# Optimization experiments

Measured on AMD Instinct MI355X. Metric: run time of the kernel, lower is better.

## Reference

```python
import jax, jax.numpy as jnp
import numpy as np

N = 50000   # nodes
E = 800000  # edges (avg degree 16)
D = 128     # in_dim == out_dim
EPS = 1e-5  # LayerNorm eps (torch default)


def setup_inputs() -> dict:
    key = jax.random.key(0)
    ks = jax.random.split(key, 8)
    x = jax.random.normal(ks[0], (N, D), dtype=jnp.float32)
    edge_row = jax.random.randint(ks[1], (E,), 0, N, dtype=jnp.int32)
    edge_col = jax.random.randint(ks[2], (E,), 0, N, dtype=jnp.int32)
    edge_val = jax.random.uniform(ks[3], (E,), dtype=jnp.float32)
    W = jax.random.normal(ks[4], (D, D), dtype=jnp.float32) / np.sqrt(D).astype(np.float32)
    b = jnp.zeros((D,), jnp.float32)
    gamma = jnp.ones((D,), jnp.float32)
    beta = jnp.zeros((D,), jnp.float32)
    return {"x": x, "edge_val": edge_val, "W": W, "b": b,
            "gamma": gamma, "beta": beta,
            "edge_row": edge_row, "edge_col": edge_col}


def reference(x, edge_val, W, b, gamma, beta, edge_row, edge_col):
    # SpMM: support = adj @ x, adj in COO form (row, col, val)
    msgs = edge_val[:, None] * x[edge_col]                      # [E, D] gather
    support = jax.ops.segment_sum(msgs, edge_row, num_segments=x.shape[0])  # [N, D]
    # Linear (torch stores weight as [out, in])
    h = support @ W.T + b                                       # [N, D]
    # LayerNorm over last dim
    mu = jnp.mean(h, axis=-1, keepdims=True)
    var = jnp.mean(jnp.square(h - mu), axis=-1, keepdims=True)
    h = (h - mu) * jax.lax.rsqrt(var + EPS) * gamma + beta
    # ReLU; dropout is identity at inference
    return jax.nn.relu(h)
```

## Files before the change

### kernel.cpp

```cpp
#include <hip/hip_runtime.h>

#define D 128
#define LN_EPS 1e-5f
#define RPB 16
#define POISON 0xAAAAAAAAu
#define BINSTRIDE 4864
#define SBF_STRIDE 68
#define ECAP 68
#define EMAX 64
#define P1BLOCKS 512
#define CURSTRIDE 16

typedef __attribute__((ext_vector_type(8))) short short8;
typedef __attribute__((ext_vector_type(4))) float f32x4;

union FragU { uint4 u; short8 s; };

__device__ __forceinline__ unsigned bf16_hi(float f) {
    unsigned u = __float_as_uint(f);
    return (u + 0x7FFFu + ((u >> 16) & 1u)) & 0xFFFF0000u;
}
__device__ __forceinline__ float lo16f(unsigned u) { return __uint_as_float(u << 16); }
__device__ __forceinline__ float hi16f(unsigned u) { return __uint_as_float(u & 0xFFFF0000u); }

__global__ void __launch_bounds__(256) prep1_kernel(
    const int* __restrict__ edge_row, const int* __restrict__ edge_col,
    const float* __restrict__ edge_val,
    const float* __restrict__ W, const float* __restrict__ x,
    unsigned* __restrict__ Wb, unsigned* __restrict__ xb16,
    unsigned* __restrict__ bin_cursor, uint2* __restrict__ binbuf,
    int E, int n8, int nbins, int epb) {
    __shared__ int cntL[256];
    __shared__ int curL[256];
    __shared__ int baseL[256];
    int t = threadIdx.x;
    int gid = blockIdx.x * 256 + t;
    int gsz = gridDim.x * 256;

    cntL[t] = 0;

    if (gid < 8192) {
        int u  = gid & 3;
        int L  = (gid >> 2) & 63;
        int nt = (gid >> 8) & 7;
        int kt = gid >> 11;
        int n = nt * 16 + (L & 15);
        int k = kt * 32 + (L >> 4) * 8 + u * 2;
        unsigned lo = bf16_hi(W[n * D + k]) >> 16;
        unsigned hi = bf16_hi(W[n * D + k + 1]);
        Wb[gid] = hi | lo;
    }

    for (int j = gid; j < n8; j += gsz) {
        float4 a = *(const float4*)(x + (size_t)j * 8);
        float4 c = *(const float4*)(x + (size_t)j * 8 + 4);
        uint4 o;
        o.x = bf16_hi(a.y) | (bf16_hi(a.x) >> 16);
        o.y = bf16_hi(a.w) | (bf16_hi(a.z) >> 16);
        o.z = bf16_hi(c.y) | (bf16_hi(c.x) >> 16);
        o.w = bf16_hi(c.w) | (bf16_hi(c.z) >> 16);
        *(uint4*)(xb16 + (size_t)j * 4) = o;
    }
    __syncthreads();

    int e0 = blockIdx.x * epb;
    int e1 = e0 + epb; if (e1 > E) e1 = E;

    {
        int i = e0 + t * 4;
        for (; i + 3 < e1; i += 1024) {
            int4 r = *(const int4*)(edge_row + i);
            atomicAdd(&cntL[r.x >> 8], 1);
            atomicAdd(&cntL[r.y >> 8], 1);
            atomicAdd(&cntL[r.z >> 8], 1);
            atomicAdd(&cntL[r.w >> 8], 1);
        }
        for (; i < e1; ++i) atomicAdd(&cntL[edge_row[i] >> 8], 1);
    }
    __syncthreads();
    if (t < nbins) {
        int c = cntL[t];
        baseL[t] = c ? (int)(atomicAdd(&bin_cursor[t * CURSTRIDE], (unsigned)c) - POISON) : 0;
    }
    curL[t] = 0;
    __syncthreads();

    {
        int i = e0 + t * 4;
        for (; i + 3 < e1; i += 1024) {
            int4 r = *(const int4*)(edge_row + i);
            int4 c = *(const int4*)(edge_col + i);
            float4 v = *(const float4*)(edge_val + i);
            int b0 = r.x >> 8, b1 = r.y >> 8, b2 = r.z >> 8, b3 = r.w >> 8;
            int p0 = atomicAdd(&curL[b0], 1) + baseL[b0];
            int p1 = atomicAdd(&curL[b1], 1) + baseL[b1];
            int p2 = atomicAdd(&curL[b2], 1) + baseL[b2];
            int p3 = atomicAdd(&curL[b3], 1) + baseL[b3];
            if (p0 < BINSTRIDE)
                binbuf[(size_t)b0 * BINSTRIDE + p0] =
                    make_uint2(((unsigned)c.x << 16) | (unsigned)(r.x & 255), bf16_hi(v.x));
            if (p1 < BINSTRIDE)
                binbuf[(size_t)b1 * BINSTRIDE + p1] =
                    make_uint2(((unsigned)c.y << 16) | (unsigned)(r.y & 255), bf16_hi(v.y));
            if (p2 < BINSTRIDE)
                binbuf[(size_t)b2 * BINSTRIDE + p2] =
                    make_uint2(((unsigned)c.z << 16) | (unsigned)(r.z & 255), bf16_hi(v.z));
            if (p3 < BINSTRIDE)
                binbuf[(size_t)b3 * BINSTRIDE + p3] =
                    make_uint2(((unsigned)c.w << 16) | (unsigned)(r.w & 255), bf16_hi(v.w));
        }
        for (; i < e1; ++i) {
            int r = edge_row[i];
            int bin = r >> 8;
            int p = atomicAdd(&curL[bin], 1) + baseL[bin];
            if (p < BINSTRIDE)
                binbuf[(size_t)bin * BINSTRIDE + p] =
                    make_uint2(((unsigned)edge_col[i] << 16) | (unsigned)(r & 255),
                               bf16_hi(edge_val[i]));
        }
    }
}

__global__ void __launch_bounds__(256) fused_gather_linear(
    const unsigned* __restrict__ xb16, const uint2* __restrict__ binbuf,
    const unsigned* __restrict__ bin_cursor, const unsigned* __restrict__ Wb,
    const float* __restrict__ b, const float* __restrict__ gamma,
    const float* __restrict__ beta, float* __restrict__ out, int N) {
    __shared__ unsigned ecol[RPB][ECAP];
    __shared__ int ecnt[RPB];
    __shared__ int pdeg[RPB];
    __shared__ unsigned sbf[RPB][SBF_STRIDE];
    __shared__ float sh[RPB][D];
    __shared__ float mu_s[RPB], inv_s[RPB];
    int t = threadIdx.x;

    int nwg = (int)gridDim.x;
    int swq = nwg >> 3, swr = nwg & 7;
    int xcd = (int)blockIdx.x & 7;
    int logical = (xcd < swr ? xcd * (swq + 1) : swr * (swq + 1) + (xcd - swr) * swq)
                + ((int)blockIdx.x >> 3);
    int row0 = logical * RPB;
    int bin  = logical >> 4;
    int tb   = (logical & 15) * RPB;

    if (t < RPB) ecnt[t] = 0;
    int sz = (int)(bin_cursor[bin * CURSTRIDE] - POISON);
    if (sz > BINSTRIDE) sz = BINSTRIDE;
    if (sz < 0) sz = 0;
    const uint2* bb = binbuf + (size_t)bin * BINSTRIDE;
    __syncthreads();

    {
        int half = sz >> 1;
        for (int i = t; i < half; i += 256) {
            uint4 two = *(const uint4*)(bb + (size_t)2 * i);
            int rl0 = (int)(two.x & 255u) - tb;
            if ((unsigned)rl0 < RPB) {
                int p = atomicAdd(&ecnt[rl0], 1);
                if (p < EMAX) ecol[rl0][p] = two.y | (two.x >> 16);
            }
            int rl1 = (int)(two.z & 255u) - tb;
            if ((unsigned)rl1 < RPB) {
                int p = atomicAdd(&ecnt[rl1], 1);
                if (p < EMAX) ecol[rl1][p] = two.w | (two.z >> 16);
            }
        }
        if (t == 0 && (sz & 1)) {
            uint2 rec = bb[sz - 1];
            int rl = (int)(rec.x & 255u) - tb;
            if ((unsigned)rl < RPB) {
                int p = atomicAdd(&ecnt[rl], 1);
                if (p < EMAX) ecol[rl][p] = rec.y | (rec.x >> 16);
            }
        }
    }
    __syncthreads();
    if (t < RPB) {
        int c = ecnt[t]; if (c > EMAX) c = EMAX;
        int pe = (c + 3) & ~3;
        for (int k = c; k < pe; ++k) ecol[t][k] = 0;
        pdeg[t] = pe;
    }
    __syncthreads();

    {
        int r = t >> 4;
        int qd = t & 15;
        int row = row0 + r;
        float4 accA = make_float4(0.f, 0.f, 0.f, 0.f);
        float4 accB = make_float4(0.f, 0.f, 0.f, 0.f);
        if (row < N) {
            int pd = pdeg[r];
            const unsigned* xb = xb16 + qd * 4;
            for (int e = 0; e < pd; e += 4) {
                uint4 p = *(const uint4*)&ecol[r][e];
                unsigned c0 = p.x & 0xFFFFu, c1 = p.y & 0xFFFFu;
                unsigned c2 = p.z & 0xFFFFu, c3 = p.w & 0xFFFFu;
                float w0 = __uint_as_float(p.x & 0xFFFF0000u);
                float w1 = __uint_as_float(p.y & 0xFFFF0000u);
                float w2 = __uint_as_float(p.z & 0xFFFF0000u);
                float w3 = __uint_as_float(p.w & 0xFFFF0000u);
                uint4 X0 = *(const uint4*)(xb + (size_t)c0 * (D / 2));
                uint4 X1 = *(const uint4*)(xb + (size_t)c1 * (D / 2));
                uint4 X2 = *(const uint4*)(xb + (size_t)c2 * (D / 2));
                uint4 X3 = *(const uint4*)(xb + (size_t)c3 * (D / 2));
                accA.x = fmaf(w0, lo16f(X0.x), accA.x);
                accA.y = fmaf(w0, hi16f(X0.x), accA.y);
                accA.z = fmaf(w0, lo16f(X0.y), accA.z);
                accA.w = fmaf(w0, hi16f(X0.y), accA.w);
                accB.x = fmaf(w0, lo16f(X0.z), accB.x);
                accB.y = fmaf(w0, hi16f(X0.z), accB.y);
                accB.z = fmaf(w0, lo16f(X0.w), accB.z);
                accB.w = fmaf(w0, hi16f(X0.w), accB.w);
                accA.x = fmaf(w1, lo16f(X1.x), accA.x);
                accA.y = fmaf(w1, hi16f(X1.x), accA.y);
                accA.z = fmaf(w1, lo16f(X1.y), accA.z);
                accA.w = fmaf(w1, hi16f(X1.y), accA.w);
                accB.x = fmaf(w1, lo16f(X1.z), accB.x);
                accB.y = fmaf(w1, hi16f(X1.z), accB.y);
                accB.z = fmaf(w1, lo16f(X1.w), accB.z);
                accB.w = fmaf(w1, hi16f(X1.w), accB.w);
                accA.x = fmaf(w2, lo16f(X2.x), accA.x);
                accA.y = fmaf(w2, hi16f(X2.x), accA.y);
                accA.z = fmaf(w2, lo16f(X2.y), accA.z);
                accA.w = fmaf(w2, hi16f(X2.y), accA.w);
                accB.x = fmaf(w2, lo16f(X2.z), accB.x);
                accB.y = fmaf(w2, hi16f(X2.z), accB.y);
                accB.z = fmaf(w2, lo16f(X2.w), accB.z);
                accB.w = fmaf(w2, hi16f(X2.w), accB.w);
                accA.x = fmaf(w3, lo16f(X3.x), accA.x);
                accA.y = fmaf(w3, hi16f(X3.x), accA.y);
                accA.z = fmaf(w3, lo16f(X3.y), accA.z);
                accA.w = fmaf(w3, hi16f(X3.y), accA.w);
                accB.x = fmaf(w3, lo16f(X3.z), accB.x);
                accB.y = fmaf(w3, hi16f(X3.z), accB.y);
                accB.z = fmaf(w3, lo16f(X3.w), accB.z);
                accB.w = fmaf(w3, hi16f(X3.w), accB.w);
            }
        }
        uint4 o;
        o.x = bf16_hi(accA.y) | (bf16_hi(accA.x) >> 16);
        o.y = bf16_hi(accA.w) | (bf16_hi(accA.z) >> 16);
        o.z = bf16_hi(accB.y) | (bf16_hi(accB.x) >> 16);
        o.w = bf16_hi(accB.w) | (bf16_hi(accB.z) >> 16);
        *(uint4*)&sbf[r][qd * 4] = o;
    }
    __syncthreads();

    {
        int L = t & 63;
        int w = t >> 6;
        int m = L & 15;
        int g = L >> 4;
        f32x4 acc0 = {0.f, 0.f, 0.f, 0.f};
        f32x4 acc1 = {0.f, 0.f, 0.f, 0.f};
#pragma unroll
        for (int kt = 0; kt < 4; ++kt) {
            FragU a, b0, b1;
            a.u  = *(const uint4*)&sbf[m][kt * 16 + g * 4];
            b0.u = *(const uint4*)(Wb + (((size_t)(kt * 8 + w * 2)) * 64 + L) * 4);
            b1.u = *(const uint4*)(Wb + (((size_t)(kt * 8 + w * 2 + 1)) * 64 + L) * 4);
            acc0 = __builtin_amdgcn_mfma_f32_16x16x32_bf16(a.s, b0.s, acc0, 0, 0, 0);
            acc1 = __builtin_amdgcn_mfma_f32_16x16x32_bf16(a.s, b1.s, acc1, 0, 0, 0);
        }
        int n0 = w * 32 + m;
        int n1 = n0 + 16;
        float bv0 = b[n0], bv1 = b[n1];
#pragma unroll
        for (int i = 0; i < 4; ++i) {
            int rr = g * 4 + i;
            sh[rr][n0] = acc0[i] + bv0;
            sh[rr][n1] = acc1[i] + bv1;
        }
    }
    __syncthreads();

    {
        int rr = t >> 4, j = t & 15;
        float sum = 0.f, sq = 0.f;
#pragma unroll
        for (int i = 0; i < 8; ++i) {
            float v = sh[rr][j + 16 * i];
            sum += v;
            sq = fmaf(v, v, sq);
        }
#pragma unroll
        for (int off = 8; off > 0; off >>= 1) {
            sum += __shfl_down(sum, off, 16);
            sq  += __shfl_down(sq, off, 16);
        }
        if (j == 0) {
            float mu = sum * (1.0f / D);
            float var = sq * (1.0f / D) - mu * mu;
            mu_s[rr] = mu;
            inv_s[rr] = rsqrtf(var + LN_EPS);
        }
    }
    __syncthreads();

    {
        int td = t & 127;
        int rbase = (t >> 7) * 8;
        float g = gamma[td], be = beta[td];
#pragma unroll
        for (int r = 0; r < 8; ++r) {
            int row = row0 + rbase + r;
            if (row < N) {
                float y = (sh[rbase + r][td] - mu_s[rbase + r]) * inv_s[rbase + r] * g + be;
                out[(size_t)row * D + td] = fmaxf(y, 0.f);
            }
        }
    }
}

extern "C" void kernel_launch(void* const* d_in, const int* in_sizes, int n_in,
                              void* d_out, int out_size, void* d_ws, size_t ws_size,
                              hipStream_t stream) {
    const float* x        = (const float*)d_in[0];
    const float* edge_val = (const float*)d_in[1];
    const float* W        = (const float*)d_in[2];
    const float* b        = (const float*)d_in[3];
    const float* gamma    = (const float*)d_in[4];
    const float* beta     = (const float*)d_in[5];
    const int*   edge_row = (const int*)d_in[6];
    const int*   edge_col = (const int*)d_in[7];

    const int N = in_sizes[0] / D;
    const int E = in_sizes[1];
    const int n8 = N * D / 8;
    const int nbins = (N + 255) >> 8;

    char* ws = (char*)d_ws;
    uint2*    binbuf     = (uint2*)ws;     ws += (size_t)nbins * BINSTRIDE * sizeof(uint2);
    unsigned* xb16       = (unsigned*)ws;  ws += (size_t)N * (D / 2) * sizeof(unsigned);
    unsigned* Wb         = (unsigned*)ws;  ws += 8192 * sizeof(unsigned);
    unsigned* bin_cursor = (unsigned*)ws;  ws += 256 * CURSTRIDE * sizeof(unsigned);

    int epb = ((E + P1BLOCKS - 1) / P1BLOCKS + 3) & ~3;

    prep1_kernel<<<P1BLOCKS, 256, 0, stream>>>(edge_row, edge_col, edge_val,
                                               W, x, Wb, xb16, bin_cursor,
                                               binbuf, E, n8, nbins, epb);
    fused_gather_linear<<<(N + RPB - 1) / RPB, 256, 0, stream>>>(
        xb16, binbuf, bin_cursor, Wb, b, gamma, beta, (float*)d_out, N);
}
```

Before: 147.2 us.

## Bucket per-row edges by column range, widen prep blocks, pad LayerNorm buffer

```diff
diff --git a/kernel.cpp b/kernel.cpp
--- a/kernel.cpp
+++ b/kernel.cpp
@@ -6,9 +6,12 @@
 #define POISON 0xAAAAAAAAu
 #define BINSTRIDE 4864
 #define SBF_STRIDE 68
+#define SH_STRIDE 132
 #define ECAP 68
 #define EMAX 64
+#define NCH 8
 #define P1BLOCKS 512
+#define P1THREADS 1024
 #define CURSTRIDE 16
 
 typedef __attribute__((ext_vector_type(8))) short short8;
@@ -23,7 +26,7 @@
 __device__ __forceinline__ float lo16f(unsigned u) { return __uint_as_float(u << 16); }
 __device__ __forceinline__ float hi16f(unsigned u) { return __uint_as_float(u & 0xFFFF0000u); }
 
-__global__ void __launch_bounds__(256) prep1_kernel(
+__global__ void __launch_bounds__(P1THREADS) prep1_kernel(
     const int* __restrict__ edge_row, const int* __restrict__ edge_col,
     const float* __restrict__ edge_val,
     const float* __restrict__ W, const float* __restrict__ x,
@@ -34,10 +37,10 @@
     __shared__ int curL[256];
     __shared__ int baseL[256];
     int t = threadIdx.x;
-    int gid = blockIdx.x * 256 + t;
-    int gsz = gridDim.x * 256;
-
-    cntL[t] = 0;
+    int gid = blockIdx.x * P1THREADS + t;
+    int gsz = gridDim.x * P1THREADS;
+
+    if (t < 256) cntL[t] = 0;
 
     if (gid < 8192) {
         int u  = gid & 3;
@@ -68,7 +71,7 @@
 
     {
         int i = e0 + t * 4;
-        for (; i + 3 < e1; i += 1024) {
+        for (; i + 3 < e1; i += P1THREADS * 4) {
             int4 r = *(const int4*)(edge_row + i);
             atomicAdd(&cntL[r.x >> 8], 1);
             atomicAdd(&cntL[r.y >> 8], 1);
@@ -82,12 +85,12 @@
         int c = cntL[t];
         baseL[t] = c ? (int)(atomicAdd(&bin_cursor[t * CURSTRIDE], (unsigned)c) - POISON) : 0;
     }
-    curL[t] = 0;
+    if (t < 256) curL[t] = 0;
     __syncthreads();
 
     {
         int i = e0 + t * 4;
-        for (; i + 3 < e1; i += 1024) {
+        for (; i + 3 < e1; i += P1THREADS * 4) {
             int4 r = *(const int4*)(edge_row + i);
             int4 c = *(const int4*)(edge_col + i);
             float4 v = *(const float4*)(edge_val + i);
@@ -127,10 +130,12 @@
     const float* __restrict__ b, const float* __restrict__ gamma,
     const float* __restrict__ beta, float* __restrict__ out, int N) {
     __shared__ unsigned ecol[RPB][ECAP];
-    __shared__ int ecnt[RPB];
+    __shared__ int cnt2[RPB][NCH];
+    __shared__ int cur2[RPB][NCH];
+    __shared__ int base2[RPB][NCH];
     __shared__ int pdeg[RPB];
     __shared__ unsigned sbf[RPB][SBF_STRIDE];
-    __shared__ float sh[RPB][D];
+    __shared__ float sh[RPB][SH_STRIDE];
     __shared__ float mu_s[RPB], inv_s[RPB];
     int t = threadIdx.x;
 
@@ -143,11 +148,42 @@
     int bin  = logical >> 4;
     int tb   = (logical & 15) * RPB;
 
-    if (t < RPB) ecnt[t] = 0;
+    if (t < RPB * NCH) {
+        ((int*)cnt2)[t] = 0;
+        ((int*)cur2)[t] = 0;
+    }
     int sz = (int)(bin_cursor[bin * CURSTRIDE] - POISON);
     if (sz > BINSTRIDE) sz = BINSTRIDE;
     if (sz < 0) sz = 0;
     const uint2* bb = binbuf + (size_t)bin * BINSTRIDE;
+    __syncthreads();
+
+    {
+        int half = sz >> 1;
+        for (int i = t; i < half; i += 256) {
+            uint4 two = *(const uint4*)(bb + (size_t)2 * i);
+            int rl0 = (int)(two.x & 255u) - tb;
+            if ((unsigned)rl0 < RPB) atomicAdd(&cnt2[rl0][two.x >> 29], 1);
+            int rl1 = (int)(two.z & 255u) - tb;
+            if ((unsigned)rl1 < RPB) atomicAdd(&cnt2[rl1][two.z >> 29], 1);
+        }
+        if (t == 0 && (sz & 1)) {
+            unsigned xw = bb[sz - 1].x;
+            int rl = (int)(xw & 255u) - tb;
+            if ((unsigned)rl < RPB) atomicAdd(&cnt2[rl][xw >> 29], 1);
+        }
+    }
+    __syncthreads();
+
+    if (t < RPB) {
+        int base = 0;
+#pragma unroll
+        for (int c = 0; c < NCH; ++c) { base2[t][c] = base; base += cnt2[t][c]; }
+        int tot = base > EMAX ? EMAX : base;
+        int pe = (tot + 3) & ~3;
+        for (int k = tot; k < pe; ++k) ecol[t][k] = 0;
+        pdeg[t] = pe;
+    }
     __syncthreads();
 
     {
@@ -156,30 +192,26 @@
             uint4 two = *(const uint4*)(bb + (size_t)2 * i);
             int rl0 = (int)(two.x & 255u) - tb;
             if ((unsigned)rl0 < RPB) {
-                int p = atomicAdd(&ecnt[rl0], 1);
-                if (p < EMAX) ecol[rl0][p] = two.y | (two.x >> 16);
+                int ch = two.x >> 29;
+                int idx = base2[rl0][ch] + atomicAdd(&cur2[rl0][ch], 1);
+                if (idx < EMAX) ecol[rl0][idx] = two.y | (two.x >> 16);
             }
             int rl1 = (int)(two.z & 255u) - tb;
             if ((unsigned)rl1 < RPB) {
-                int p = atomicAdd(&ecnt[rl1], 1);
-                if (p < EMAX) ecol[rl1][p] = two.w | (two.z >> 16);
+                int ch = two.z >> 29;
+                int idx = base2[rl1][ch] + atomicAdd(&cur2[rl1][ch], 1);
+                if (idx < EMAX) ecol[rl1][idx] = two.w | (two.z >> 16);
             }
         }
         if (t == 0 && (sz & 1)) {
             uint2 rec = bb[sz - 1];
             int rl = (int)(rec.x & 255u) - tb;
             if ((unsigned)rl < RPB) {
-                int p = atomicAdd(&ecnt[rl], 1);
-                if (p < EMAX) ecol[rl][p] = rec.y | (rec.x >> 16);
-            }
-        }
-    }
-    __syncthreads();
-    if (t < RPB) {
-        int c = ecnt[t]; if (c > EMAX) c = EMAX;
-        int pe = (c + 3) & ~3;
-        for (int k = c; k < pe; ++k) ecol[t][k] = 0;
-        pdeg[t] = pe;
+                int ch = rec.x >> 29;
+                int idx = base2[rl][ch] + atomicAdd(&cur2[rl][ch], 1);
+                if (idx < EMAX) ecol[rl][idx] = rec.y | (rec.x >> 16);
+            }
+        }
     }
     __syncthreads();
 
@@ -338,9 +370,9 @@
 
     int epb = ((E + P1BLOCKS - 1) / P1BLOCKS + 3) & ~3;
 
-    prep1_kernel<<<P1BLOCKS, 256, 0, stream>>>(edge_row, edge_col, edge_val,
-                                               W, x, Wb, xb16, bin_cursor,
-                                               binbuf, E, n8, nbins, epb);
+    prep1_kernel<<<P1BLOCKS, P1THREADS, 0, stream>>>(edge_row, edge_col, edge_val,
+                                                     W, x, Wb, xb16, bin_cursor,
+                                                     binbuf, E, n8, nbins, epb);
     fused_gather_linear<<<(N + RPB - 1) / RPB, 256, 0, stream>>>(
         xb16, binbuf, bin_cursor, Wb, b, gamma, beta, (float*)d_out, N);
 }
```

After: 155.8 us. 1.06x slower.

## Sort edges per block in shared memory before coalesced bin scatter; prefetch gather

Applied to the files above, without the earlier changes.

```diff
diff --git a/kernel.cpp b/kernel.cpp
--- a/kernel.cpp
+++ b/kernel.cpp
@@ -6,9 +6,12 @@
 #define POISON 0xAAAAAAAAu
 #define BINSTRIDE 4864
 #define SBF_STRIDE 68
+#define SH_STRIDE 132
 #define ECAP 68
 #define EMAX 64
 #define P1BLOCKS 512
+#define P1THREADS 1024
+#define DENSECAP 1600
 #define CURSTRIDE 16
 
 typedef __attribute__((ext_vector_type(8))) short short8;
@@ -23,7 +26,7 @@
 __device__ __forceinline__ float lo16f(unsigned u) { return __uint_as_float(u << 16); }
 __device__ __forceinline__ float hi16f(unsigned u) { return __uint_as_float(u & 0xFFFF0000u); }
 
-__global__ void __launch_bounds__(256) prep1_kernel(
+__global__ void __launch_bounds__(P1THREADS) prep1_kernel(
     const int* __restrict__ edge_row, const int* __restrict__ edge_col,
     const float* __restrict__ edge_val,
     const float* __restrict__ W, const float* __restrict__ x,
@@ -32,12 +35,15 @@
     int E, int n8, int nbins, int epb) {
     __shared__ int cntL[256];
     __shared__ int curL[256];
-    __shared__ int baseL[256];
+    __shared__ int lbaseL[256];
+    __shared__ int gbaseL[256];
+    __shared__ int tmp[2][256];
+    __shared__ uint2 dense[DENSECAP];
     int t = threadIdx.x;
-    int gid = blockIdx.x * 256 + t;
-    int gsz = gridDim.x * 256;
-
-    cntL[t] = 0;
+    int gid = blockIdx.x * P1THREADS + t;
+    int gsz = gridDim.x * P1THREADS;
+
+    if (t < 256) cntL[t] = 0;
 
     if (gid < 8192) {
         int u  = gid & 3;
@@ -65,10 +71,11 @@
 
     int e0 = blockIdx.x * epb;
     int e1 = e0 + epb; if (e1 > E) e1 = E;
+    int nume = e1 - e0; if (nume < 0) nume = 0;
 
     {
         int i = e0 + t * 4;
-        for (; i + 3 < e1; i += 1024) {
+        for (; i + 3 < e1; i += P1THREADS * 4) {
             int4 r = *(const int4*)(edge_row + i);
             atomicAdd(&cntL[r.x >> 8], 1);
             atomicAdd(&cntL[r.y >> 8], 1);
@@ -78,46 +85,66 @@
         for (; i < e1; ++i) atomicAdd(&cntL[edge_row[i] >> 8], 1);
     }
     __syncthreads();
+
     if (t < nbins) {
         int c = cntL[t];
-        baseL[t] = c ? (int)(atomicAdd(&bin_cursor[t * CURSTRIDE], (unsigned)c) - POISON) : 0;
-    }
-    curL[t] = 0;
+        gbaseL[t] = c ? (int)(atomicAdd(&bin_cursor[t * CURSTRIDE], (unsigned)c) - POISON) : 0;
+    }
+    if (t < 256) tmp[0][t] = cntL[t];
+    __syncthreads();
+    int buf = 0;
+    for (int off = 1; off < 256; off <<= 1) {
+        if (t < 256) {
+            int v = tmp[buf][t];
+            if (t >= off) v += tmp[buf][t - off];
+            tmp[1 - buf][t] = v;
+        }
+        buf ^= 1;
+        __syncthreads();
+    }
+    if (t < 256) {
+        lbaseL[t] = tmp[buf][t] - cntL[t];
+        curL[t] = 0;
+    }
     __syncthreads();
 
     {
         int i = e0 + t * 4;
-        for (; i + 3 < e1; i += 1024) {
+        for (; i + 3 < e1; i += P1THREADS * 4) {
             int4 r = *(const int4*)(edge_row + i);
             int4 c = *(const int4*)(edge_col + i);
             float4 v = *(const float4*)(edge_val + i);
             int b0 = r.x >> 8, b1 = r.y >> 8, b2 = r.z >> 8, b3 = r.w >> 8;
-            int p0 = atomicAdd(&curL[b0], 1) + baseL[b0];
-            int p1 = atomicAdd(&curL[b1], 1) + baseL[b1];
-            int p2 = atomicAdd(&curL[b2], 1) + baseL[b2];
-            int p3 = atomicAdd(&curL[b3], 1) + baseL[b3];
-            if (p0 < BINSTRIDE)
-                binbuf[(size_t)b0 * BINSTRIDE + p0] =
-                    make_uint2(((unsigned)c.x << 16) | (unsigned)(r.x & 255), bf16_hi(v.x));
-            if (p1 < BINSTRIDE)
-                binbuf[(size_t)b1 * BINSTRIDE + p1] =
-                    make_uint2(((unsigned)c.y << 16) | (unsigned)(r.y & 255), bf16_hi(v.y));
-            if (p2 < BINSTRIDE)
-                binbuf[(size_t)b2 * BINSTRIDE + p2] =
-                    make_uint2(((unsigned)c.z << 16) | (unsigned)(r.z & 255), bf16_hi(v.z));
-            if (p3 < BINSTRIDE)
-                binbuf[(size_t)b3 * BINSTRIDE + p3] =
-                    make_uint2(((unsigned)c.w << 16) | (unsigned)(r.w & 255), bf16_hi(v.w));
+            int p0 = atomicAdd(&curL[b0], 1) + lbaseL[b0];
+            int p1 = atomicAdd(&curL[b1], 1) + lbaseL[b1];
+            int p2 = atomicAdd(&curL[b2], 1) + lbaseL[b2];
+            int p3 = atomicAdd(&curL[b3], 1) + lbaseL[b3];
+            dense[p0] = make_uint2(((unsigned)c.x << 16) | (unsigned)(r.x & 255),
+                                   bf16_hi(v.x) | (unsigned)b0);
+            dense[p1] = make_uint2(((unsigned)c.y << 16) | (unsigned)(r.y & 255),
+                                   bf16_hi(v.y) | (unsigned)b1);
+            dense[p2] = make_uint2(((unsigned)c.z << 16) | (unsigned)(r.z & 255),
+                                   bf16_hi(v.z) | (unsigned)b2);
+            dense[p3] = make_uint2(((unsigned)c.w << 16) | (unsigned)(r.w & 255),
+                                   bf16_hi(v.w) | (unsigned)b3);
         }
         for (; i < e1; ++i) {
             int r = edge_row[i];
             int bin = r >> 8;
-            int p = atomicAdd(&curL[bin], 1) + baseL[bin];
-            if (p < BINSTRIDE)
-                binbuf[(size_t)bin * BINSTRIDE + p] =
-                    make_uint2(((unsigned)edge_col[i] << 16) | (unsigned)(r & 255),
-                               bf16_hi(edge_val[i]));
-        }
+            int p = atomicAdd(&curL[bin], 1) + lbaseL[bin];
+            dense[p] = make_uint2(((unsigned)edge_col[i] << 16) | (unsigned)(r & 255),
+                                  bf16_hi(edge_val[i]) | (unsigned)bin);
+        }
+    }
+    __syncthreads();
+
+    for (int i = t; i < nume; i += P1THREADS) {
+        uint2 rec = dense[i];
+        int bin = (int)(rec.y & 255u);
+        int pos = gbaseL[bin] + (i - lbaseL[bin]);
+        if (pos < BINSTRIDE)
+            binbuf[(size_t)bin * BINSTRIDE + pos] =
+                make_uint2(rec.x, rec.y & 0xFFFF0000u);
     }
 }
 
@@ -130,7 +157,7 @@
     __shared__ int ecnt[RPB];
     __shared__ int pdeg[RPB];
     __shared__ unsigned sbf[RPB][SBF_STRIDE];
-    __shared__ float sh[RPB][D];
+    __shared__ float sh[RPB][SH_STRIDE];
     __shared__ float mu_s[RPB], inv_s[RPB];
     int t = threadIdx.x;
 
@@ -192,50 +219,61 @@
         if (row < N) {
             int pd = pdeg[r];
             const unsigned* xb = xb16 + qd * 4;
-            for (int e = 0; e < pd; e += 4) {
-                uint4 p = *(const uint4*)&ecol[r][e];
-                unsigned c0 = p.x & 0xFFFFu, c1 = p.y & 0xFFFFu;
-                unsigned c2 = p.z & 0xFFFFu, c3 = p.w & 0xFFFFu;
-                float w0 = __uint_as_float(p.x & 0xFFFF0000u);
-                float w1 = __uint_as_float(p.y & 0xFFFF0000u);
-                float w2 = __uint_as_float(p.z & 0xFFFF0000u);
-                float w3 = __uint_as_float(p.w & 0xFFFF0000u);
-                uint4 X0 = *(const uint4*)(xb + (size_t)c0 * (D / 2));
-                uint4 X1 = *(const uint4*)(xb + (size_t)c1 * (D / 2));
-                uint4 X2 = *(const uint4*)(xb + (size_t)c2 * (D / 2));
-                uint4 X3 = *(const uint4*)(xb + (size_t)c3 * (D / 2));
-                accA.x = fmaf(w0, lo16f(X0.x), accA.x);
-                accA.y = fmaf(w0, hi16f(X0.x), accA.y);
-                accA.z = fmaf(w0, lo16f(X0.y), accA.z);
-                accA.w = fmaf(w0, hi16f(X0.y), accA.w);
-                accB.x = fmaf(w0, lo16f(X0.z), accB.x);
-                accB.y = fmaf(w0, hi16f(X0.z), accB.y);
-                accB.z = fmaf(w0, lo16f(X0.w), accB.z);
-                accB.w = fmaf(w0, hi16f(X0.w), accB.w);
-                accA.x = fmaf(w1, lo16f(X1.x), accA.x);
-                accA.y = fmaf(w1, hi16f(X1.x), accA.y);
-                accA.z = fmaf(w1, lo16f(X1.y), accA.z);
-                accA.w = fmaf(w1, hi16f(X1.y), accA.w);
-                accB.x = fmaf(w1, lo16f(X1.z), accB.x);
-                accB.y = fmaf(w1, hi16f(X1.z), accB.y);
-                accB.z = fmaf(w1, lo16f(X1.w), accB.z);
-                accB.w = fmaf(w1, hi16f(X1.w), accB.w);
-                accA.x = fmaf(w2, lo16f(X2.x), accA.x);
-                accA.y = fmaf(w2, hi16f(X2.x), accA.y);
-                accA.z = fmaf(w2, lo16f(X2.y), accA.z);
-                accA.w = fmaf(w2, hi16f(X2.y), accA.w);
-                accB.x = fmaf(w2, lo16f(X2.z), accB.x);
-                accB.y = fmaf(w2, hi16f(X2.z), accB.y);
-                accB.z = fmaf(w2, lo16f(X2.w), accB.z);
-                accB.w = fmaf(w2, hi16f(X2.w), accB.w);
-                accA.x = fmaf(w3, lo16f(X3.x), accA.x);
-                accA.y = fmaf(w3, hi16f(X3.x), accA.y);
-                accA.z = fmaf(w3, lo16f(X3.y), accA.z);
-                accA.w = fmaf(w3, hi16f(X3.y), accA.w);
-                accB.x = fmaf(w3, lo16f(X3.z), accB.x);
-                accB.y = fmaf(w3, hi16f(X3.z), accB.y);
-                accB.z = fmaf(w3, lo16f(X3.w), accB.z);
-                accB.w = fmaf(w3, hi16f(X3.w), accB.w);
+            if (pd > 0) {
+                uint4 p = *(const uint4*)&ecol[r][0];
+                uint4 X0 = *(const uint4*)(xb + (size_t)(p.x & 0xFFFFu) * (D / 2));
+                uint4 X1 = *(const uint4*)(xb + (size_t)(p.y & 0xFFFFu) * (D / 2));
+                uint4 X2 = *(const uint4*)(xb + (size_t)(p.z & 0xFFFFu) * (D / 2));
+                uint4 X3 = *(const uint4*)(xb + (size_t)(p.w & 0xFFFFu) * (D / 2));
+                for (int e = 4;; e += 4) {
+                    uint4 pn, Y0, Y1, Y2, Y3;
+                    bool more = e < pd;
+                    if (more) {
+                        pn = *(const uint4*)&ecol[r][e];
+                        Y0 = *(const uint4*)(xb + (size_t)(pn.x & 0xFFFFu) * (D / 2));
+                        Y1 = *(const uint4*)(xb + (size_t)(pn.y & 0xFFFFu) * (D / 2));
+                        Y2 = *(const uint4*)(xb + (size_t)(pn.z & 0xFFFFu) * (D / 2));
+                        Y3 = *(const uint4*)(xb + (size_t)(pn.w & 0xFFFFu) * (D / 2));
+                    }
+                    float w0 = __uint_as_float(p.x & 0xFFFF0000u);
+                    float w1 = __uint_as_float(p.y & 0xFFFF0000u);
+                    float w2 = __uint_as_float(p.z & 0xFFFF0000u);
+                    float w3 = __uint_as_float(p.w & 0xFFFF0000u);
+                    accA.x = fmaf(w0, lo16f(X0.x), accA.x);
+                    accA.y = fmaf(w0, hi16f(X0.x), accA.y);
+                    accA.z = fmaf(w0, lo16f(X0.y), accA.z);
+                    accA.w = fmaf(w0, hi16f(X0.y), accA.w);
+                    accB.x = fmaf(w0, lo16f(X0.z), accB.x);
+                    accB.y = fmaf(w0, hi16f(X0.z), accB.y);
+                    accB.z = fmaf(w0, lo16f(X0.w), accB.z);
+                    accB.w = fmaf(w0, hi16f(X0.w), accB.w);
+                    accA.x = fmaf(w1, lo16f(X1.x), accA.x);
+                    accA.y = fmaf(w1, hi16f(X1.x), accA.y);
+                    accA.z = fmaf(w1, lo16f(X1.y), accA.z);
+                    accA.w = fmaf(w1, hi16f(X1.y), accA.w);
+                    accB.x = fmaf(w1, lo16f(X1.z), accB.x);
+                    accB.y = fmaf(w1, hi16f(X1.z), accB.y);
+                    accB.z = fmaf(w1, lo16f(X1.w), accB.z);
+                    accB.w = fmaf(w1, hi16f(X1.w), accB.w);
+                    accA.x = fmaf(w2, lo16f(X2.x), accA.x);
+                    accA.y = fmaf(w2, hi16f(X2.x), accA.y);
+                    accA.z = fmaf(w2, lo16f(X2.y), accA.z);
+                    accA.w = fmaf(w2, hi16f(X2.y), accA.w);
+                    accB.x = fmaf(w2, lo16f(X2.z), accB.x);
+                    accB.y = fmaf(w2, hi16f(X2.z), accB.y);
+                    accB.z = fmaf(w2, lo16f(X2.w), accB.z);
+                    accB.w = fmaf(w2, hi16f(X2.w), accB.w);
+                    accA.x = fmaf(w3, lo16f(X3.x), accA.x);
+                    accA.y = fmaf(w3, hi16f(X3.x), accA.y);
+                    accA.z = fmaf(w3, lo16f(X3.y), accA.z);
+                    accA.w = fmaf(w3, hi16f(X3.y), accA.w);
+                    accB.x = fmaf(w3, lo16f(X3.z), accB.x);
+                    accB.y = fmaf(w3, hi16f(X3.z), accB.y);
+                    accB.z = fmaf(w3, lo16f(X3.w), accB.z);
+                    accB.w = fmaf(w3, hi16f(X3.w), accB.w);
+                    if (!more) break;
+                    p = pn; X0 = Y0; X1 = Y1; X2 = Y2; X3 = Y3;
+                }
             }
         }
         uint4 o;
@@ -338,9 +376,9 @@
 
     int epb = ((E + P1BLOCKS - 1) / P1BLOCKS + 3) & ~3;
 
-    prep1_kernel<<<P1BLOCKS, 256, 0, stream>>>(edge_row, edge_col, edge_val,
-                                               W, x, Wb, xb16, bin_cursor,
-                                               binbuf, E, n8, nbins, epb);
+    prep1_kernel<<<P1BLOCKS, P1THREADS, 0, stream>>>(edge_row, edge_col, edge_val,
+                                                     W, x, Wb, xb16, bin_cursor,
+                                                     binbuf, E, n8, nbins, epb);
     fused_gather_linear<<<(N + RPB - 1) / RPB, 256, 0, stream>>>(
         xb16, binbuf, bin_cursor, Wb, b, gamma, beta, (float*)d_out, N);
 }
```

Measured after the change: 147.7 us. Within noise of the previous version (+0.3%).
